# Kernel optimization log

Measured on AMD Instinct MI355X. Metric: run time of the kernel, lower is better.

Reference implementation:

```python
import jax, jax.numpy as jnp
import numpy as np

B, T, D, H = 2, 2048, 1024, 16
HD = D // H
EPS = 1e-5


def setup_inputs() -> dict:
    key = jax.random.key(0)
    ks = jax.random.split(key, 6)
    scale = 0.02
    return {
        "x": jax.random.normal(ks[0], (B, T, D), dtype=jnp.float32),
        "wq": jax.random.normal(ks[1], (D, D), dtype=jnp.float32) * scale,
        "bq": jnp.zeros((D,), dtype=jnp.float32),
        "wk": jax.random.normal(ks[2], (D, D), dtype=jnp.float32) * scale,
        "bk": jnp.zeros((D,), dtype=jnp.float32),
        "wv": jax.random.normal(ks[3], (D, D), dtype=jnp.float32) * scale,
        "bv": jnp.zeros((D,), dtype=jnp.float32),
        "wg": jax.random.normal(ks[4], (D, D), dtype=jnp.float32) * scale,
        "bg": jnp.zeros((D,), dtype=jnp.float32),
        "gamma": jnp.ones((D,), dtype=jnp.float32),
        "beta": jnp.zeros((D,), dtype=jnp.float32),
    }


def reference(x, wq, bq, wk, bk, wv, bv, wg, bg, gamma, beta):
    b, t, d = x.shape
    # projections (torch Linear: y = x @ W^T + b, W stored as (out, in))
    def proj(w, bias):
        return jnp.einsum('btd,ed->bte', x, w) + bias
    q = proj(wq, bq).reshape(b, t, H, HD).swapaxes(1, 2)  # b h t hd
    k = proj(wk, bk).reshape(b, t, H, HD).swapaxes(1, 2)
    v = proj(wv, bv).reshape(b, t, H, HD).swapaxes(1, 2)
    # full (non-causal) attention as in the source
    scores = jnp.einsum('bhqd,bhkd->bhqk', q, k) / jnp.sqrt(jnp.float32(HD))
    attn = jax.nn.softmax(scores, axis=-1)
    out = jnp.einsum('bhqk,bhkd->bhqd', attn, v)
    out = out.swapaxes(1, 2).reshape(b, t, d)  # b t (h hd)
    gate = proj(wg, bg)
    y = gate * out
    # GroupNorm with n_heads groups over the channel (d_model) dim, per token
    yg = y.reshape(b, t, H, HD)
    mu = jnp.mean(yg, axis=-1, keepdims=True)
    var = jnp.var(yg, axis=-1, keepdims=True)
    yn = (yg - mu) / jnp.sqrt(var + EPS)
    yn = yn * gamma.reshape(H, HD) + beta.reshape(H, HD)
    return yn.reshape(b, t, d)
```

## Files before the change

### kernel.cpp

```cpp
#include <hip/hip_runtime.h>
#include <hip/hip_bf16.h>
#include <math.h>

namespace {
constexpr int kB = 2, kT = 2048, kD = 1024, kH = 16, kHD = 64;
}

typedef __attribute__((ext_vector_type(8))) short short8;
typedef __attribute__((ext_vector_type(4))) float f32x4;
typedef __attribute__((ext_vector_type(16))) float f32x16;

#if __has_builtin(__builtin_amdgcn_exp2f)
#define EXP2F(x) __builtin_amdgcn_exp2f(x)
#else
#define EXP2F(x) __expf((x) * 0.6931471805599453f)
#endif

__device__ __forceinline__ ushort f2bf(float f) {
  union { float f; uint u; } c; c.f = f;
  uint u = c.u + 0x7FFFu + ((c.u >> 16) & 1u);
  return (ushort)(u >> 16);
}

__device__ __forceinline__ float bf2f(ushort u) {
  union { uint u; float f; } c; c.u = ((uint)u) << 16; return c.f;
}

__device__ __forceinline__ uint pack_bf2(float a, float b) {
  uint r;
  asm("v_cvt_pk_bf16_f32 %0, %1, %2" : "=v"(r) : "v"(a), "v"(b));
  return r;
}

__device__ __forceinline__ void gload_lds16(const void* g, void* l) {
  __builtin_amdgcn_global_load_lds(
      (const __attribute__((address_space(1))) void*)g,
      (__attribute__((address_space(3))) void*)l, 16, 0, 0);
}

__global__ __launch_bounds__(256) void cvt_kernel(
    const float* __restrict__ x, const float* __restrict__ w0,
    const float* __restrict__ w1, const float* __restrict__ w2,
    const float* __restrict__ w3, ushort* __restrict__ out)
{
  const size_t g = (size_t)blockIdx.x * 256 + threadIdx.x;
  const size_t e = g * 4;
  const float* src; size_t rel;
  if (e < ((size_t)1 << 22)) { src = x; rel = e; }
  else {
    size_t e2 = e - ((size_t)1 << 22);
    int wi = (int)(e2 >> 20);
    src = wi == 0 ? w0 : wi == 1 ? w1 : wi == 2 ? w2 : w3;
    rel = e2 & (((size_t)1 << 20) - 1);
  }
  float4 v = *reinterpret_cast<const float4*>(src + rel);
  ushort4 u;
  u.x = f2bf(v.x); u.y = f2bf(v.y); u.z = f2bf(v.z); u.w = f2bf(v.w);
  *reinterpret_cast<ushort4*>(out + e) = u;
}

__device__ __forceinline__ void stage_half(
    const ushort* __restrict__ src, int row0, int kcol0,
    ushort* ldsbase, int wid, int lane)
{
#pragma unroll
  for (int part = 0; part < 2; ++part) {
    const int c = part * 512 + wid * 64 + lane;
    const int x = c * 16;
    const int o = x ^ (((x >> 7) & 3) << 4);
    const int r = o >> 6;
    const int cb = (o & 63) >> 1;
    gload_lds16(src + (size_t)(row0 + r) * kD + kcol0 + cb, ldsbase + (x >> 1));
  }
}

__device__ __forceinline__ short8 read_frag(const ushort* half, int r, int lg) {
  const int slot = lg ^ ((r >> 1) & 3);
  return *reinterpret_cast<const short8*>(&half[r * 32 + slot * 8]);
}

#define PH_BAR() do { asm volatile("" ::: "memory"); \
  __builtin_amdgcn_s_barrier(); asm volatile("" ::: "memory"); } while (0)

__global__ __launch_bounds__(512, 2) void proj_mfma_kernel(
    const ushort* __restrict__ Xb, const ushort* __restrict__ Wb,
    const float* __restrict__ bq, const float* __restrict__ bk,
    const float* __restrict__ bv, const float* __restrict__ bg,
    ushort* __restrict__ qo, ushort* __restrict__ ko,
    ushort* __restrict__ vt, ushort* __restrict__ go)
{
  const int mat = blockIdx.z;
  const ushort* Wm = Wb + (size_t)mat * 1024 * 1024;
  const float* bias = mat == 0 ? bq : mat == 1 ? bk : mat == 2 ? bv : bg;
  const int m0 = blockIdx.x * 256;
  const int n0g = blockIdx.y * 256;
  const int tid = threadIdx.x;
  const int wid = tid >> 6, lane = tid & 63;
  const int wr = wid >> 2, wc = wid & 3;
  const int wrow = wr * 128, wcol = wc * 64;
  const int lr = lane & 15, lg = lane >> 4;

  __shared__ ushort lds[65536];

  f32x4 acc[8][4];
#pragma unroll
  for (int i = 0; i < 8; ++i)
#pragma unroll
    for (int j = 0; j < 4; ++j) acc[i][j] = (f32x4){0.f, 0.f, 0.f, 0.f};

  short8 bfr[4];

#define STAGE_A(bu, h, kt) stage_half(Xb, m0,  (kt) * 64 + (h) * 32, \
    &lds[(bu) * 32768 + (h) * 8192], wid, lane)
#define STAGE_B(bu, h, kt) stage_half(Wm, n0g, (kt) * 64 + (h) * 32, \
    &lds[(bu) * 32768 + 16384 + (h) * 8192], wid, lane)

#define PHASE(bu, h, MB, READB, STAGE_STMT, DOVM)                          \
  {                                                                        \
    const ushort* Ah = &lds[(bu) * 32768 + (h) * 8192];                    \
    const ushort* Bh = &lds[(bu) * 32768 + 16384 + (h) * 8192];            \
    short8 af[4];                                                          \
    af[0] = read_frag(Ah, wrow + (MB + 0) * 16 + lr, lg);                  \
    af[1] = read_frag(Ah, wrow + (MB + 1) * 16 + lr, lg);                  \
    af[2] = read_frag(Ah, wrow + (MB + 2) * 16 + lr, lg);                  \
    af[3] = read_frag(Ah, wrow + (MB + 3) * 16 + lr, lg);                  \
    if (READB) {                                                           \
      bfr[0] = read_frag(Bh, wcol + 0 * 16 + lr, lg);                      \
      bfr[1] = read_frag(Bh, wcol + 1 * 16 + lr, lg);                      \
      bfr[2] = read_frag(Bh, wcol + 2 * 16 + lr, lg);                      \
      bfr[3] = read_frag(Bh, wcol + 3 * 16 + lr, lg);                      \
    }                                                                      \
    STAGE_STMT;                                                            \
    PH_BAR();                                                              \
    __builtin_amdgcn_s_setprio(1);                                         \
    _Pragma("unroll")                                                      \
    for (int m2 = 0; m2 < 4; ++m2)                                         \
      _Pragma("unroll")                                                    \
      for (int ni = 0; ni < 4; ++ni)                                       \
        acc[(MB) + m2][ni] = __builtin_amdgcn_mfma_f32_16x16x32_bf16(      \
            af[m2], bfr[ni], acc[(MB) + m2][ni], 0, 0, 0);                 \
    __builtin_amdgcn_s_setprio(0);                                         \
    if (DOVM) asm volatile("s_waitcnt vmcnt(4)" ::: "memory");             \
    PH_BAR();                                                              \
  }

  STAGE_A(0, 0, 0); STAGE_B(0, 0, 0);
  STAGE_A(0, 1, 0); STAGE_B(0, 1, 0);
  STAGE_A(1, 0, 1); STAGE_B(1, 0, 1);
  asm volatile("s_waitcnt vmcnt(4)" ::: "memory");
  PH_BAR();

#pragma unroll 1
  for (int it = 0; it < 8; ++it) {
    const int ta = 2 * it, tb = 2 * it + 1;
    const int tn0 = (ta + 2) & 15;
    const int tn1 = (tb + 2) & 15;
    PHASE(0, 0, 0, 1, (STAGE_A(1, 1, tb)),  0)
    PHASE(0, 0, 4, 0, (STAGE_B(1, 1, tb)),  0)
    PHASE(0, 1, 0, 1, (STAGE_A(0, 0, tn0)), 0)
    PHASE(0, 1, 4, 0, (STAGE_B(0, 0, tn0)), 1)
    PHASE(1, 0, 0, 1, (STAGE_A(0, 1, tn0)), 0)
    PHASE(1, 0, 4, 0, (STAGE_B(0, 1, tn0)), 0)
    PHASE(1, 1, 0, 1, (STAGE_A(1, 0, tn1)), 0)
    PHASE(1, 1, 4, 0, (STAGE_B(1, 0, tn1)), 1)
  }

#undef PHASE
#undef STAGE_A
#undef STAGE_B

  const float vsc = (mat == 0) ? 0.18033688f : 1.0f;

#pragma unroll
  for (int mi = 0; mi < 8; ++mi) {
    const int mbase = m0 + wrow + mi * 16 + 4 * lg;
    const int b = mbase >> 11, t0r = mbase & (kT - 1);
#pragma unroll
    for (int ni = 0; ni < 4; ++ni) {
      const int n = n0g + wcol + ni * 16 + lr;
      const float bn = bias[n];
      if (mat == 3) {
#pragma unroll
        for (int r = 0; r < 4; ++r)
          go[(size_t)(mbase + r) * kD + n] = f2bf(acc[mi][ni][r] + bn);
      } else if (mat == 2) {
        const int h = n >> 6, hd = n & 63;
        const int bh = b * kH + h;
        const int nh = hd >> 5, lv = hd & 31;
        const int kc = t0r >> 5, kk0 = t0r & 31;
        const int jf = kk0 >> 4, hi2 = (kk0 >> 3) & 1, jj0 = kk0 & 7;
        const int lane2 = lv + hi2 * 32;
        const size_t off =
            (((((size_t)bh * 64 + kc) * 2 + nh) * 2 + jf) * 64 + lane2) * 8 + jj0;
        ushort4 u;
        u.x = f2bf(acc[mi][ni][0] + bn); u.y = f2bf(acc[mi][ni][1] + bn);
        u.z = f2bf(acc[mi][ni][2] + bn); u.w = f2bf(acc[mi][ni][3] + bn);
        *reinterpret_cast<ushort4*>(&vt[off]) = u;
      } else {
        const int h = n >> 6, hd = n & 63;
        const int bh = b * kH + h;
        const int hk = hd >> 4, hi2 = (hd >> 3) & 1, jj = hd & 7;
        ushort* dst = (mat == 0) ? qo : ko;
#pragma unroll
        for (int r = 0; r < 4; ++r) {
          const int t = t0r + r;
          const int kc = t >> 5, kk = t & 31;
          const size_t off =
              ((((size_t)bh * 64 + kc) * 4 + hk) * 64 + kk + hi2 * 32) * 8 + jj;
          dst[off] = f2bf((acc[mi][ni][r] + bn) * vsc);
        }
      }
    }
  }
}

__global__ __launch_bounds__(256, 4) void attn_mfma32_kernel(
    const ushort* __restrict__ Qf, const ushort* __restrict__ Kf,
    const ushort* __restrict__ Vf, ushort* __restrict__ Op,
    float* __restrict__ lsumP)
{
  const int bid = blockIdx.x;
  const int xcd = bid & 7;
  const int j = bid >> 3;
  const int bh = xcd * 4 + (j >> 6);
  const int rem = j & 63;
  const int qt = rem & 15;
  const int ks = rem >> 4;
  const int tid = threadIdx.x, w = tid >> 6, lane = tid & 63;
  const int lq = lane & 31;
  const int hi = lane >> 5;

  __shared__ ushort kvA[4096];
  __shared__ ushort kvB[4096];

  const ushort* qfp = Qf + (((size_t)bh * 64 + (qt * 4 + w)) * 4) * 512;
  short8 aq[4];
#pragma unroll
  for (int hk = 0; hk < 4; ++hk)
    aq[hk] = *reinterpret_cast<const short8*>(&qfp[((size_t)hk * 64 + lane) * 8]);

  f32x16 oacc[2];
#pragma unroll
  for (int nh = 0; nh < 2; ++nh)
#pragma unroll
    for (int r = 0; r < 16; ++r) oacc[nh][r] = 0.f;
  float lsum = 0.f;

  const ushort* kbase = Kf + ((size_t)bh * 64 + ks * 16) * 2048;
  const ushort* vbase = Vf + ((size_t)bh * 64 + ks * 16) * 2048;

#define STAGE_KV(dst, t) do {                                               \
    gload_lds16(kbase + (size_t)(t) * 2048 + tid * 8, &dst[tid * 8]);       \
    gload_lds16(vbase + (size_t)(t) * 2048 + tid * 8, &dst[2048 + tid * 8]);\
  } while (0)

#define COMPUTE_KV(buf) do {                                                \
    short8 kf_[4];                                                          \
    _Pragma("unroll")                                                       \
    for (int hk = 0; hk < 4; ++hk)                                          \
      kf_[hk] = *reinterpret_cast<const short8*>(&buf[(hk * 64 + lane) * 8]);\
    short8 vf[2][2];                                                        \
    _Pragma("unroll")                                                       \
    for (int nh = 0; nh < 2; ++nh)                                          \
      _Pragma("unroll")                                                     \
      for (int jf = 0; jf < 2; ++jf)                                        \
        vf[nh][jf] = *reinterpret_cast<const short8*>(                      \
            &buf[2048 + ((nh * 2 + jf) * 64 + lane) * 8]);                  \
    f32x16 s;                                                               \
    _Pragma("unroll")                                                       \
    for (int r = 0; r < 16; ++r) s[r] = 0.f;                                \
    __builtin_amdgcn_s_setprio(1);                                          \
    _Pragma("unroll")                                                       \
    for (int hk = 0; hk < 4; ++hk)                                          \
      s = __builtin_amdgcn_mfma_f32_32x32x16_bf16(kf_[hk], aq[hk], s, 0, 0, 0);\
    __builtin_amdgcn_s_setprio(0);                                          \
    float p[16];                                                            \
    _Pragma("unroll")                                                       \
    for (int r = 0; r < 16; ++r) p[r] = EXP2F(s[r]);                        \
    float t0 = 0.f, t1 = 0.f;                                               \
    _Pragma("unroll")                                                       \
    for (int r = 0; r < 16; r += 2) { t0 += p[r]; t1 += p[r + 1]; }         \
    lsum += t0 + t1;                                                        \
    uint pk[8];                                                             \
    _Pragma("unroll")                                                       \
    for (int m = 0; m < 8; ++m) pk[m] = pack_bf2(p[2 * m], p[2 * m + 1]);   \
    union { uint u[4]; short8 s8; } fa0, fa1;                               \
    {                                                                       \
      auto s0 = __builtin_amdgcn_permlane32_swap(pk[0], pk[2], false, false);\
      auto s1 = __builtin_amdgcn_permlane32_swap(pk[1], pk[3], false, false);\
      auto s2 = __builtin_amdgcn_permlane32_swap(pk[4], pk[6], false, false);\
      auto s3 = __builtin_amdgcn_permlane32_swap(pk[5], pk[7], false, false);\
      fa0.u[0] = s0[0]; fa0.u[2] = s0[1];                                   \
      fa0.u[1] = s1[0]; fa0.u[3] = s1[1];                                   \
      fa1.u[0] = s2[0]; fa1.u[2] = s2[1];                                   \
      fa1.u[1] = s3[0]; fa1.u[3] = s3[1];                                   \
    }                                                                       \
    __builtin_amdgcn_s_setprio(1);                                          \
    oacc[0] = __builtin_amdgcn_mfma_f32_32x32x16_bf16(vf[0][0], fa0.s8, oacc[0], 0, 0, 0);\
    oacc[0] = __builtin_amdgcn_mfma_f32_32x32x16_bf16(vf[0][1], fa1.s8, oacc[0], 0, 0, 0);\
    oacc[1] = __builtin_amdgcn_mfma_f32_32x32x16_bf16(vf[1][0], fa0.s8, oacc[1], 0, 0, 0);\
    oacc[1] = __builtin_amdgcn_mfma_f32_32x32x16_bf16(vf[1][1], fa1.s8, oacc[1], 0, 0, 0);\
    __builtin_amdgcn_s_setprio(0);                                          \
  } while (0)

  STAGE_KV(kvA, 0);
  __syncthreads();

#pragma unroll 1
  for (int kt = 0; kt < 16; kt += 2) {
    if (kt + 1 < 16) STAGE_KV(kvB, kt + 1);
    COMPUTE_KV(kvA);
    __syncthreads();
    if (kt + 2 < 16) STAGE_KV(kvA, kt + 2);
    COMPUTE_KV(kvB);
    __syncthreads();
  }

#undef STAGE_KV
#undef COMPUTE_KV

  lsum += __shfl_xor(lsum, 32);

  const int q0 = qt * 128 + w * 32;
  const size_t prow = (((size_t)ks * 32 + bh) * kT + (q0 + lq)) * kHD;
#pragma unroll
  for (int nh = 0; nh < 2; ++nh)
#pragma unroll
    for (int g2 = 0; g2 < 4; ++g2) {
      ushort4 u;
      u.x = f2bf(oacc[nh][4 * g2 + 0]);
      u.y = f2bf(oacc[nh][4 * g2 + 1]);
      u.z = f2bf(oacc[nh][4 * g2 + 2]);
      u.w = f2bf(oacc[nh][4 * g2 + 3]);
      *reinterpret_cast<ushort4*>(&Op[prow + nh * 32 + 8 * g2 + 4 * hi]) = u;
    }
  if (hi == 0)
    lsumP[((size_t)ks * 32 + bh) * kT + q0 + lq] = lsum;
}

__global__ __launch_bounds__(256) void gn_kernel(
    const ushort* __restrict__ gb, const ushort* __restrict__ Op,
    const float* __restrict__ lsumP,
    const float* __restrict__ gamma, const float* __restrict__ beta,
    float* __restrict__ out)
{
  const int grp = blockIdx.x * 4 + (threadIdx.x >> 6);
  const int lane = threadIdx.x & 63;
  const int bt = grp >> 4, h = grp & 15;
  const int b = bt >> 11, t = bt & (kT - 1);
  const int bh = b * kH + h;

  float o_un = 0.f, l = 0.f;
#pragma unroll
  for (int ks = 0; ks < 4; ++ks) {
    const size_t base = ((size_t)ks * 32 + bh) * kT + t;
    o_un += bf2f(Op[base * kHD + lane]);
    l += lsumP[base];
  }
  const float o = o_un / l;
  const float y = bf2f(gb[(size_t)bt * kD + h * kHD + lane]) * o;

  float s = y, ss = y * y;
#pragma unroll
  for (int off = 32; off; off >>= 1) {
    s  += __shfl_xor(s, off);
    ss += __shfl_xor(ss, off);
  }
  const float mean = s * (1.f / 64.f);
  const float var  = ss * (1.f / 64.f) - mean * mean;
  const float inv  = rsqrtf(var + 1e-5f);
  out[(size_t)bt * kD + h * kHD + lane] =
      (y - mean) * inv * gamma[h * kHD + lane] + beta[h * kHD + lane];
}

extern "C" void kernel_launch(void* const* d_in, const int* in_sizes, int n_in,
                              void* d_out, int out_size, void* d_ws, size_t ws_size,
                              hipStream_t stream) {
  const float* x     = (const float*)d_in[0];
  const float* wq    = (const float*)d_in[1];
  const float* bq    = (const float*)d_in[2];
  const float* wk    = (const float*)d_in[3];
  const float* bk    = (const float*)d_in[4];
  const float* wv    = (const float*)d_in[5];
  const float* bv    = (const float*)d_in[6];
  const float* wg    = (const float*)d_in[7];
  const float* bg    = (const float*)d_in[8];
  const float* gamma = (const float*)d_in[9];
  const float* beta  = (const float*)d_in[10];

  ushort* cb  = (ushort*)d_ws;
  ushort* qb  = cb + (size_t)8388608;
  ushort* kb  = qb + (size_t)4194304;
  ushort* vtb = kb + (size_t)4194304;
  ushort* gb  = vtb + (size_t)4194304;
  ushort* Op  = gb + (size_t)4194304;
  float*  lsumP = (float*)cb;
  float*  out = (float*)d_out;

  const ushort* xb = cb;
  const ushort* wb = cb + (size_t)4194304;

  cvt_kernel<<<8192, 256, 0, stream>>>(x, wq, wk, wv, wg, cb);
  proj_mfma_kernel<<<dim3(16, 4, 4), 512, 0, stream>>>(
      xb, wb, bq, bk, bv, bg, qb, kb, vtb, gb);
  attn_mfma32_kernel<<<2048, 256, 0, stream>>>(qb, kb, vtb, Op, lsumP);
  gn_kernel<<<16384, 256, 0, stream>>>(gb, Op, lsumP, gamma, beta, out);
}
```

Baseline: 109.9 us.

## Store Q/K row-major and V transposed; vectorize group-norm kernel

```diff
diff --git a/kernel.cpp b/kernel.cpp
--- a/kernel.cpp
+++ b/kernel.cpp
@@ -185,38 +185,28 @@
           go[(size_t)(mbase + r) * kD + n] = f2bf(acc[mi][ni][r] + bn);
       } else if (mat == 2) {
         const int h = n >> 6, hd = n & 63;
-        const int bh = b * kH + h;
-        const int nh = hd >> 5, lv = hd & 31;
-        const int kc = t0r >> 5, kk0 = t0r & 31;
-        const int jf = kk0 >> 4, hi2 = (kk0 >> 3) & 1, jj0 = kk0 & 7;
-        const int lane2 = lv + hi2 * 32;
-        const size_t off =
-            (((((size_t)bh * 64 + kc) * 2 + nh) * 2 + jf) * 64 + lane2) * 8 + jj0;
+        const int bh2 = b * kH + h;
         ushort4 u;
         u.x = f2bf(acc[mi][ni][0] + bn); u.y = f2bf(acc[mi][ni][1] + bn);
         u.z = f2bf(acc[mi][ni][2] + bn); u.w = f2bf(acc[mi][ni][3] + bn);
-        *reinterpret_cast<ushort4*>(&vt[off]) = u;
+        *reinterpret_cast<ushort4*>(
+            &vt[((size_t)bh2 * kHD + hd) * kT + t0r]) = u;
       } else {
         const int h = n >> 6, hd = n & 63;
-        const int bh = b * kH + h;
-        const int hk = hd >> 4, hi2 = (hd >> 3) & 1, jj = hd & 7;
+        const int bh2 = b * kH + h;
         ushort* dst = (mat == 0) ? qo : ko;
 #pragma unroll
-        for (int r = 0; r < 4; ++r) {
-          const int t = t0r + r;
-          const int kc = t >> 5, kk = t & 31;
-          const size_t off =
-              ((((size_t)bh * 64 + kc) * 4 + hk) * 64 + kk + hi2 * 32) * 8 + jj;
-          dst[off] = f2bf((acc[mi][ni][r] + bn) * vsc);
-        }
+        for (int r = 0; r < 4; ++r)
+          dst[((size_t)bh2 * kT + t0r + r) * kHD + hd] =
+              f2bf((acc[mi][ni][r] + bn) * vsc);
       }
     }
   }
 }
 
 __global__ __launch_bounds__(256, 4) void attn_mfma32_kernel(
-    const ushort* __restrict__ Qf, const ushort* __restrict__ Kf,
-    const ushort* __restrict__ Vf, ushort* __restrict__ Op,
+    const ushort* __restrict__ Qrm, const ushort* __restrict__ Krm,
+    const ushort* __restrict__ Vtr, ushort* __restrict__ Op,
     float* __restrict__ lsumP)
 {
   const int bid = blockIdx.x;
@@ -233,11 +223,12 @@
   __shared__ ushort kvA[4096];
   __shared__ ushort kvB[4096];
 
-  const ushort* qfp = Qf + (((size_t)bh * 64 + (qt * 4 + w)) * 4) * 512;
+  const int q0 = qt * 128 + w * 32;
   short8 aq[4];
 #pragma unroll
   for (int hk = 0; hk < 4; ++hk)
-    aq[hk] = *reinterpret_cast<const short8*>(&qfp[((size_t)hk * 64 + lane) * 8]);
+    aq[hk] = *reinterpret_cast<const short8*>(
+        &Qrm[((size_t)bh * kT + q0 + lq) * kHD + hk * 16 + hi * 8]);
 
   f32x16 oacc[2];
 #pragma unroll
@@ -246,12 +237,14 @@
     for (int r = 0; r < 16; ++r) oacc[nh][r] = 0.f;
   float lsum = 0.f;
 
-  const ushort* kbase = Kf + ((size_t)bh * 64 + ks * 16) * 2048;
-  const ushort* vbase = Vf + ((size_t)bh * 64 + ks * 16) * 2048;
+  const size_t koff = ((size_t)bh * kT + ks * 512 + (tid & 31)) * kHD
+                      + (tid >> 6) * 16 + ((tid >> 5) & 1) * 8;
+  const size_t voff = ((size_t)bh * kHD + (tid >> 7) * 32 + (tid & 31)) * kT
+                      + ks * 512 + ((tid >> 6) & 1) * 16 + ((tid >> 5) & 1) * 8;
 
 #define STAGE_KV(dst, t) do {                                               \
-    gload_lds16(kbase + (size_t)(t) * 2048 + tid * 8, &dst[tid * 8]);       \
-    gload_lds16(vbase + (size_t)(t) * 2048 + tid * 8, &dst[2048 + tid * 8]);\
+    gload_lds16(Krm + koff + (size_t)(t) * (32 * kHD), &dst[tid * 8]);      \
+    gload_lds16(Vtr + voff + (size_t)(t) * 32, &dst[2048 + tid * 8]);       \
   } while (0)
 
 #define COMPUTE_KV(buf) do {                                                \
@@ -321,7 +314,6 @@
 
   lsum += __shfl_xor(lsum, 32);
 
-  const int q0 = qt * 128 + w * 32;
   const size_t prow = (((size_t)ks * 32 + bh) * kT + (q0 + lq)) * kHD;
 #pragma unroll
   for (int nh = 0; nh < 2; ++nh)
@@ -344,33 +336,49 @@
     const float* __restrict__ gamma, const float* __restrict__ beta,
     float* __restrict__ out)
 {
-  const int grp = blockIdx.x * 4 + (threadIdx.x >> 6);
-  const int lane = threadIdx.x & 63;
+  const int tid = threadIdx.x;
+  const int grp = blockIdx.x * 16 + (tid >> 4);
+  const int l16 = tid & 15;
   const int bt = grp >> 4, h = grp & 15;
   const int b = bt >> 11, t = bt & (kT - 1);
   const int bh = b * kH + h;
-
-  float o_un = 0.f, l = 0.f;
+  const int c0 = l16 * 4;
+
+  float l = 0.f;
+  float ov[4] = {0.f, 0.f, 0.f, 0.f};
 #pragma unroll
   for (int ks = 0; ks < 4; ++ks) {
     const size_t base = ((size_t)ks * 32 + bh) * kT + t;
-    o_un += bf2f(Op[base * kHD + lane]);
+    ushort4 o4 = *reinterpret_cast<const ushort4*>(&Op[base * kHD + c0]);
+    ov[0] += bf2f(o4.x); ov[1] += bf2f(o4.y);
+    ov[2] += bf2f(o4.z); ov[3] += bf2f(o4.w);
     l += lsumP[base];
   }
-  const float o = o_un / l;
-  const float y = bf2f(gb[(size_t)bt * kD + h * kHD + lane]) * o;
-
-  float s = y, ss = y * y;
-#pragma unroll
-  for (int off = 32; off; off >>= 1) {
+  const float inv_l = 1.f / l;
+  ushort4 g4 = *reinterpret_cast<const ushort4*>(&gb[(size_t)bt * kD + h * kHD + c0]);
+  float y[4];
+  y[0] = bf2f(g4.x) * ov[0] * inv_l; y[1] = bf2f(g4.y) * ov[1] * inv_l;
+  y[2] = bf2f(g4.z) * ov[2] * inv_l; y[3] = bf2f(g4.w) * ov[3] * inv_l;
+
+  float s = y[0] + y[1] + y[2] + y[3];
+  float ss = y[0]*y[0] + y[1]*y[1] + y[2]*y[2] + y[3]*y[3];
+#pragma unroll
+  for (int off = 8; off; off >>= 1) {
     s  += __shfl_xor(s, off);
     ss += __shfl_xor(ss, off);
   }
   const float mean = s * (1.f / 64.f);
   const float var  = ss * (1.f / 64.f) - mean * mean;
   const float inv  = rsqrtf(var + 1e-5f);
-  out[(size_t)bt * kD + h * kHD + lane] =
-      (y - mean) * inv * gamma[h * kHD + lane] + beta[h * kHD + lane];
+
+  float4 gm = *reinterpret_cast<const float4*>(&gamma[h * kHD + c0]);
+  float4 bt4 = *reinterpret_cast<const float4*>(&beta[h * kHD + c0]);
+  float4 o;
+  o.x = (y[0] - mean) * inv * gm.x + bt4.x;
+  o.y = (y[1] - mean) * inv * gm.y + bt4.y;
+  o.z = (y[2] - mean) * inv * gm.z + bt4.z;
+  o.w = (y[3] - mean) * inv * gm.w + bt4.w;
+  *reinterpret_cast<float4*>(&out[(size_t)bt * kD + h * kHD + c0]) = o;
 }
 
 extern "C" void kernel_launch(void* const* d_in, const int* in_sizes, int n_in,
@@ -404,5 +412,5 @@
   proj_mfma_kernel<<<dim3(16, 4, 4), 512, 0, stream>>>(
       xb, wb, bq, bk, bv, bg, qb, kb, vtb, gb);
   attn_mfma32_kernel<<<2048, 256, 0, stream>>>(qb, kb, vtb, Op, lsumP);
-  gn_kernel<<<16384, 256, 0, stream>>>(gb, Op, lsumP, gamma, beta, out);
-}
+  gn_kernel<<<4096, 256, 0, stream>>>(gb, Op, lsumP, gamma, beta, out);
+}
```

Measured after the change: 111.2 us. About the same (+1.2%).
